# Kernel optimization log

Hardware: AMD Instinct MI355X
Metric: run time of the kernel (lower is better)

## Reference

```python
import jax, jax.numpy as jnp
import numpy as np

N_NODES = 50000
N_EDGES = 800000
D_IN = 128
D_OUT = 128


def setup_inputs() -> dict:
    key = jax.random.key(0)
    ks = jax.random.split(key, 10)
    x = jax.random.normal(ks[0], (N_NODES, D_IN), dtype=jnp.float32)
    lp_rows = jax.random.randint(ks[1], (N_EDGES,), 0, N_NODES, dtype=jnp.int32)
    lp_cols = jax.random.randint(ks[2], (N_EDGES,), 0, N_NODES, dtype=jnp.int32)
    # low-pass operator: positive normalized-adjacency-like weights
    lp_vals = jax.random.uniform(ks[3], (N_EDGES,), dtype=jnp.float32) / 16.0
    hp_rows = jax.random.randint(ks[4], (N_EDGES,), 0, N_NODES, dtype=jnp.int32)
    hp_cols = jax.random.randint(ks[5], (N_EDGES,), 0, N_NODES, dtype=jnp.int32)
    # high-pass operator: signed (Laplacian-like) weights
    hp_vals = jax.random.normal(ks[6], (N_EDGES,), dtype=jnp.float32) / 16.0
    alpha_w = jax.random.normal(ks[7], (1, D_IN), dtype=jnp.float32) * 0.05
    alpha_b = jnp.zeros((1,), dtype=jnp.float32)
    W = jax.random.normal(ks[8], (D_OUT, D_IN), dtype=jnp.float32) * (1.0 / np.sqrt(D_IN))
    b = jnp.zeros((D_OUT,), dtype=jnp.float32)
    return {"x": x, "lp_rows": lp_rows, "lp_cols": lp_cols, "lp_vals": lp_vals,
            "hp_rows": hp_rows, "hp_cols": hp_cols, "hp_vals": hp_vals,
            "alpha_w": alpha_w, "alpha_b": alpha_b, "W": W, "b": b}


def _spmm(rows, cols, vals, x, n):
    # COO sparse-dense matmul: out[r] += vals[e] * x[cols[e]]
    return jax.ops.segment_sum(vals[:, None] * x[cols], rows, num_segments=n)


def reference(x, lp_rows, lp_cols, lp_vals, hp_rows, hp_cols, hp_vals,
              alpha_w, alpha_b, W, b):
    n = x.shape[0]
    # per-node mixing gate: alpha_i = sigmoid(x_i . theta + b)  -> [N, 1]
    alpha = jax.nn.sigmoid(x @ alpha_w.T + alpha_b)
    z_lp = _spmm(lp_rows, lp_cols, lp_vals, x, n)   # [N, D_IN]
    z_hp = _spmm(hp_rows, hp_cols, hp_vals, x, n)   # [N, D_IN]
    z_mix = alpha * z_lp + (1.0 - alpha) * z_hp
    out = jax.nn.relu(z_mix @ W.T + b)              # use_activation=True
    return out, alpha
```

## Files before the change

kernel.cpp:

```cpp
#include <hip/hip_runtime.h>

#define N_NODES_C 50000
#define N_EDGES_C 800000
#define N_EDGES2_C (2 * N_EDGES_C)
#define D 128
#define NSHARD 8
#define OFCAP 4096

#define BROWS 4
#define NBKT (N_NODES_C / BROWS)
#define NSB (NSHARD * NBKT)
#define BCAP 32

#define GNODES 64
#define LDP 132
#define GGRID ((N_NODES_C + GNODES - 1) / GNODES)
#define FGRID 2048
#define FEPB ((N_EDGES2_C + FGRID - 1) / FGRID)
#define TOTG (GGRID + FGRID)

static __device__ __forceinline__ unsigned short f2bf(float f) {
  unsigned u = __float_as_uint(f);
  u += 0x7fff + ((u >> 16) & 1);
  return (unsigned short)(u >> 16);
}
static __device__ __forceinline__ float bf_lo(unsigned u) {
  return __uint_as_float(u << 16);
}
static __device__ __forceinline__ float bf_hi(unsigned u) {
  return __uint_as_float(u & 0xffff0000u);
}

static __device__ __forceinline__ int xcd_id() {
  int v;
  asm volatile("s_getreg_b32 %0, hwreg(HW_REG_XCC_ID, 0, 4)" : "=s"(v));
  return v & (NSHARD - 1);
}

__global__ __launch_bounds__(256) void alpha_zero_kernel(
    const float* __restrict__ x,
    const float* __restrict__ aw,
    const float* __restrict__ ab,
    float* __restrict__ alpha_out,
    float* __restrict__ alpha_ws,
    int* __restrict__ bcursor,
    int n) {
  int gtid = blockIdx.x * blockDim.x + threadIdx.x;
  if (gtid < NSB + 64) bcursor[gtid] = 0;

  int wave = gtid >> 6;
  int lane = threadIdx.x & 63;
  if (wave >= n) return;
  const float* xr = x + (size_t)wave * D;
  float s = xr[lane] * aw[lane] + xr[lane + 64] * aw[lane + 64];
  #pragma unroll
  for (int off = 32; off > 0; off >>= 1)
    s += __shfl_down(s, off);
  if (lane == 0) {
    float a = 1.0f / (1.0f + __expf(-(s + ab[0])));
    alpha_out[wave] = a;
    alpha_ws[wave] = a;
  }
}

__global__ __launch_bounds__(256) void gemm_fill_kernel(
    const float* __restrict__ x,
    const float* __restrict__ W,
    unsigned* __restrict__ y,
    const int* __restrict__ lp_rows, const int* __restrict__ lp_cols,
    const float* __restrict__ lp_vals,
    const int* __restrict__ hp_rows, const int* __restrict__ hp_cols,
    const float* __restrict__ hp_vals,
    const float* __restrict__ alpha,
    int* __restrict__ bcursor,
    uint2* __restrict__ bins,
    int* __restrict__ ofcnt,
    uint2* __restrict__ ofl,
    int n) {
  __shared__ float zs[GNODES][LDP];
  __shared__ float wt[64][LDP];

  int t = threadIdx.x;
  int bid = blockIdx.x;
  int g = (bid * GGRID) / TOTG;
  int gn = ((bid + 1) * GGRID) / TOTG;

  if (gn > g) {
    int node0 = g * GNODES;
    int tn = t & 15;
    int tjg = t >> 4;
    int jb = tjg * 4;

    #pragma unroll
    for (int it = 0; it < 8; ++it) {
      int f = t + it * 256;
      int r = f >> 5;
      int c4 = f & 31;
      int node = node0 + r;
      float4 v = make_float4(0.f, 0.f, 0.f, 0.f);
      if (node < n) v = ((const float4*)(x + (size_t)node * D))[c4];
      *(float4*)&zs[r][c4 * 4] = v;
    }

    for (int jh = 0; jh < 2; ++jh) {
      if (jh) __syncthreads();
      #pragma unroll
      for (int it = 0; it < 8; ++it) {
        int f = t + it * 256;
        int j = f >> 5;
        int k4 = f & 31;
        *(float4*)&wt[j][k4 * 4] =
            ((const float4*)W)[(size_t)(jh * 64 + j) * 32 + k4];
      }
      __syncthreads();

      float acc[4][4] = {};
      #pragma unroll 2
      for (int k = 0; k < D; k += 4) {
        float4 w0 = *(const float4*)&wt[jb + 0][k];
        float4 w1 = *(const float4*)&wt[jb + 1][k];
        float4 w2 = *(const float4*)&wt[jb + 2][k];
        float4 w3 = *(const float4*)&wt[jb + 3][k];
        float4 z0 = *(const float4*)&zs[tn][k];
        float4 z1 = *(const float4*)&zs[tn + 16][k];
        float4 z2 = *(const float4*)&zs[tn + 32][k];
        float4 z3 = *(const float4*)&zs[tn + 48][k];
        acc[0][0] += z0.x*w0.x + z0.y*w0.y + z0.z*w0.z + z0.w*w0.w;
        acc[0][1] += z0.x*w1.x + z0.y*w1.y + z0.z*w1.z + z0.w*w1.w;
        acc[0][2] += z0.x*w2.x + z0.y*w2.y + z0.z*w2.z + z0.w*w2.w;
        acc[0][3] += z0.x*w3.x + z0.y*w3.y + z0.z*w3.z + z0.w*w3.w;
        acc[1][0] += z1.x*w0.x + z1.y*w0.y + z1.z*w0.z + z1.w*w0.w;
        acc[1][1] += z1.x*w1.x + z1.y*w1.y + z1.z*w1.z + z1.w*w1.w;
        acc[1][2] += z1.x*w2.x + z1.y*w2.y + z1.z*w2.z + z1.w*w2.w;
        acc[1][3] += z1.x*w3.x + z1.y*w3.y + z1.z*w3.z + z1.w*w3.w;
        acc[2][0] += z2.x*w0.x + z2.y*w0.y + z2.z*w0.z + z2.w*w0.w;
        acc[2][1] += z2.x*w1.x + z2.y*w1.y + z2.z*w1.z + z2.w*w1.w;
        acc[2][2] += z2.x*w2.x + z2.y*w2.y + z2.z*w2.z + z2.w*w2.w;
        acc[2][3] += z2.x*w3.x + z2.y*w3.y + z2.z*w3.z + z2.w*w3.w;
        acc[3][0] += z3.x*w0.x + z3.y*w0.y + z3.z*w0.z + z3.w*w0.w;
        acc[3][1] += z3.x*w1.x + z3.y*w1.y + z3.z*w1.z + z3.w*w1.w;
        acc[3][2] += z3.x*w2.x + z3.y*w2.y + z3.z*w2.z + z3.w*w2.w;
        acc[3][3] += z3.x*w3.x + z3.y*w3.y + z3.z*w3.z + z3.w*w3.w;
      }

      #pragma unroll
      for (int ii = 0; ii < 4; ++ii) {
        int node = node0 + ii * 16 + tn;
        if (node < n) {
          uint2 o;
          o.x = (unsigned)f2bf(acc[ii][0]) | ((unsigned)f2bf(acc[ii][1]) << 16);
          o.y = (unsigned)f2bf(acc[ii][2]) | ((unsigned)f2bf(acc[ii][3]) << 16);
          *(uint2*)&y[(size_t)node * 64 + jh * 32 + tjg * 2] = o;
        }
      }
    }
  } else {
    int fb = bid - g;
    int xcc = xcd_id();
    int e0 = fb * FEPB;
    int e1 = e0 + FEPB;
    if (e1 > N_EDGES2_C) e1 = N_EDGES2_C;
    for (int e = e0 + t; e < e1; e += 256) {
      int r, c;
      float v;
      if (e < N_EDGES_C) {
        r = __builtin_nontemporal_load(lp_rows + e);
        c = __builtin_nontemporal_load(lp_cols + e);
        v = __builtin_nontemporal_load(lp_vals + e) * alpha[r];
      } else {
        int i = e - N_EDGES_C;
        r = __builtin_nontemporal_load(hp_rows + i);
        c = __builtin_nontemporal_load(hp_cols + i);
        v = __builtin_nontemporal_load(hp_vals + i) * (1.0f - alpha[r]);
      }
      int sb = xcc * NBKT + (r >> 2);
      int p = atomicAdd(&bcursor[sb], 1);
      if (p < BCAP) {
        bins[(size_t)sb * BCAP + p] =
            make_uint2(((unsigned)r << 16) | (unsigned)c, __float_as_uint(v));
      } else {
        int q = atomicAdd(ofcnt, 1);
        if (q < OFCAP)
          ofl[q] = make_uint2(((unsigned)r << 16) | (unsigned)c,
                              (unsigned)__float_as_int(v));
      }
    }
  }
}

__global__ __launch_bounds__(256) void gather_kernel(
    const int* __restrict__ bcursor,
    const uint2* __restrict__ bins,
    const unsigned* __restrict__ y,
    const float* __restrict__ bias,
    const int* __restrict__ ofcnt,
    const uint2* __restrict__ ofl,
    float* __restrict__ out) {
  int t = threadIdx.x;
  int w = t >> 6;
  int lane = t & 63;
  int bkt = blockIdx.x * 4 + w;

  float a0L = 0.f, a0H = 0.f, a1L = 0.f, a1H = 0.f;
  float a2L = 0.f, a2H = 0.f, a3L = 0.f, a3H = 0.f;

  #define ACC(RR, VV, UU)                                        \
    do {                                                         \
      float uL_ = bf_lo(UU), uH_ = bf_hi(UU);                    \
      switch (RR) {                                              \
        case 0: a0L += (VV) * uL_; a0H += (VV) * uH_; break;     \
        case 1: a1L += (VV) * uL_; a1H += (VV) * uH_; break;     \
        case 2: a2L += (VV) * uL_; a2H += (VV) * uH_; break;     \
        default: a3L += (VV) * uL_; a3H += (VV) * uH_; break;    \
      }                                                          \
    } while (0)

  int cnts[8];
  uint2 wvs[8];
  #pragma unroll
  for (int s = 0; s < 8; ++s) {
    int c = bcursor[s * NBKT + bkt];
    cnts[s] = c > BCAP ? BCAP : c;
  }
  #pragma unroll
  for (int s = 0; s < 8; ++s) {
    wvs[s] = make_uint2(0u, 0u);
    if (lane < cnts[s])
      wvs[s] = bins[(size_t)(s * NBKT + bkt) * BCAP + lane];
  }

  #pragma unroll
  for (int s = 0; s < 8; ++s) {
    int cnt = cnts[s];
    uint2 wv = wvs[s];
    int i = 0;
    for (; i + 7 < cnt; i += 8) {
      unsigned xk0 = (unsigned)__shfl((int)wv.x, i + 0);
      unsigned xk1 = (unsigned)__shfl((int)wv.x, i + 1);
      unsigned xk2 = (unsigned)__shfl((int)wv.x, i + 2);
      unsigned xk3 = (unsigned)__shfl((int)wv.x, i + 3);
      unsigned xk4 = (unsigned)__shfl((int)wv.x, i + 4);
      unsigned xk5 = (unsigned)__shfl((int)wv.x, i + 5);
      unsigned xk6 = (unsigned)__shfl((int)wv.x, i + 6);
      unsigned xk7 = (unsigned)__shfl((int)wv.x, i + 7);
      float v0 = __uint_as_float((unsigned)__shfl((int)wv.y, i + 0));
      float v1 = __uint_as_float((unsigned)__shfl((int)wv.y, i + 1));
      float v2 = __uint_as_float((unsigned)__shfl((int)wv.y, i + 2));
      float v3 = __uint_as_float((unsigned)__shfl((int)wv.y, i + 3));
      float v4 = __uint_as_float((unsigned)__shfl((int)wv.y, i + 4));
      float v5 = __uint_as_float((unsigned)__shfl((int)wv.y, i + 5));
      float v6 = __uint_as_float((unsigned)__shfl((int)wv.y, i + 6));
      float v7 = __uint_as_float((unsigned)__shfl((int)wv.y, i + 7));
      unsigned u0 = y[(size_t)(xk0 & 0xffffu) * 64 + lane];
      unsigned u1 = y[(size_t)(xk1 & 0xffffu) * 64 + lane];
      unsigned u2 = y[(size_t)(xk2 & 0xffffu) * 64 + lane];
      unsigned u3 = y[(size_t)(xk3 & 0xffffu) * 64 + lane];
      unsigned u4 = y[(size_t)(xk4 & 0xffffu) * 64 + lane];
      unsigned u5 = y[(size_t)(xk5 & 0xffffu) * 64 + lane];
      unsigned u6 = y[(size_t)(xk6 & 0xffffu) * 64 + lane];
      unsigned u7 = y[(size_t)(xk7 & 0xffffu) * 64 + lane];
      int r0 = (int)__builtin_amdgcn_readfirstlane((xk0 >> 16) & 3);
      int r1 = (int)__builtin_amdgcn_readfirstlane((xk1 >> 16) & 3);
      int r2 = (int)__builtin_amdgcn_readfirstlane((xk2 >> 16) & 3);
      int r3 = (int)__builtin_amdgcn_readfirstlane((xk3 >> 16) & 3);
      int r4 = (int)__builtin_amdgcn_readfirstlane((xk4 >> 16) & 3);
      int r5 = (int)__builtin_amdgcn_readfirstlane((xk5 >> 16) & 3);
      int r6 = (int)__builtin_amdgcn_readfirstlane((xk6 >> 16) & 3);
      int r7 = (int)__builtin_amdgcn_readfirstlane((xk7 >> 16) & 3);
      ACC(r0, v0, u0);
      ACC(r1, v1, u1);
      ACC(r2, v2, u2);
      ACC(r3, v3, u3);
      ACC(r4, v4, u4);
      ACC(r5, v5, u5);
      ACC(r6, v6, u6);
      ACC(r7, v7, u7);
    }
    for (; i + 3 < cnt; i += 4) {
      unsigned xk0 = (unsigned)__shfl((int)wv.x, i + 0);
      unsigned xk1 = (unsigned)__shfl((int)wv.x, i + 1);
      unsigned xk2 = (unsigned)__shfl((int)wv.x, i + 2);
      unsigned xk3 = (unsigned)__shfl((int)wv.x, i + 3);
      float v0 = __uint_as_float((unsigned)__shfl((int)wv.y, i + 0));
      float v1 = __uint_as_float((unsigned)__shfl((int)wv.y, i + 1));
      float v2 = __uint_as_float((unsigned)__shfl((int)wv.y, i + 2));
      float v3 = __uint_as_float((unsigned)__shfl((int)wv.y, i + 3));
      unsigned u0 = y[(size_t)(xk0 & 0xffffu) * 64 + lane];
      unsigned u1 = y[(size_t)(xk1 & 0xffffu) * 64 + lane];
      unsigned u2 = y[(size_t)(xk2 & 0xffffu) * 64 + lane];
      unsigned u3 = y[(size_t)(xk3 & 0xffffu) * 64 + lane];
      int r0 = (int)__builtin_amdgcn_readfirstlane((xk0 >> 16) & 3);
      int r1 = (int)__builtin_amdgcn_readfirstlane((xk1 >> 16) & 3);
      int r2 = (int)__builtin_amdgcn_readfirstlane((xk2 >> 16) & 3);
      int r3 = (int)__builtin_amdgcn_readfirstlane((xk3 >> 16) & 3);
      ACC(r0, v0, u0);
      ACC(r1, v1, u1);
      ACC(r2, v2, u2);
      ACC(r3, v3, u3);
    }
    for (; i < cnt; ++i) {
      unsigned xk0 = (unsigned)__shfl((int)wv.x, i);
      float v0 = __uint_as_float((unsigned)__shfl((int)wv.y, i));
      unsigned u0 = y[(size_t)(xk0 & 0xffffu) * 64 + lane];
      int r0 = (int)__builtin_amdgcn_readfirstlane((xk0 >> 16) & 3);
      ACC(r0, v0, u0);
    }
  }

  int nof = *ofcnt;
  if (nof > OFCAP) nof = OFCAP;
  for (int i = 0; i < nof; ++i) {
    uint2 o = ofl[i];
    unsigned r = o.x >> 16;
    if ((int)(r >> 2) == bkt) {
      unsigned u = y[(size_t)(o.x & 0xffffu) * 64 + lane];
      float v = __uint_as_float(o.y);
      ACC((int)(r & 3), v, u);
    }
  }
  #undef ACC

  float2 bv = *(const float2*)&bias[lane * 2];
  size_t ro = (size_t)bkt * 4 * D + lane * 2;
  float2 o0, o1, o2, o3;
  o0.x = fmaxf(a0L + bv.x, 0.0f); o0.y = fmaxf(a0H + bv.y, 0.0f);
  o1.x = fmaxf(a1L + bv.x, 0.0f); o1.y = fmaxf(a1H + bv.y, 0.0f);
  o2.x = fmaxf(a2L + bv.x, 0.0f); o2.y = fmaxf(a2H + bv.y, 0.0f);
  o3.x = fmaxf(a3L + bv.x, 0.0f); o3.y = fmaxf(a3H + bv.y, 0.0f);
  *(float2*)&out[ro + 0 * D] = o0;
  *(float2*)&out[ro + 1 * D] = o1;
  *(float2*)&out[ro + 2 * D] = o2;
  *(float2*)&out[ro + 3 * D] = o3;
}

extern "C" void kernel_launch(void* const* d_in, const int* in_sizes, int n_in,
                              void* d_out, int out_size, void* d_ws, size_t ws_size,
                              hipStream_t stream) {
  const float* x = (const float*)d_in[0];
  const int* lp_rows = (const int*)d_in[1];
  const int* lp_cols = (const int*)d_in[2];
  const float* lp_vals = (const float*)d_in[3];
  const int* hp_rows = (const int*)d_in[4];
  const int* hp_cols = (const int*)d_in[5];
  const float* hp_vals = (const float*)d_in[6];
  const float* alpha_w = (const float*)d_in[7];
  const float* alpha_b = (const float*)d_in[8];
  const float* W = (const float*)d_in[9];
  const float* bias = (const float*)d_in[10];

  float* out = (float*)d_out;
  float* alpha_out = out + (size_t)N_NODES_C * D;

  char* ws = (char*)d_ws;
  unsigned* y = (unsigned*)ws;   ws += (size_t)N_NODES_C * 64 * 4;
  float* alpha_ws = (float*)ws;  ws += 200192;
  int* bcursor = (int*)ws;       ws += (size_t)NSB * 4;
  int* ofcnt = (int*)ws;         ws += 256;
  uint2* ofl = (uint2*)ws;       ws += (size_t)OFCAP * 8;
  uint2* bins = (uint2*)ws;
  ws += (size_t)NSB * BCAP * 8;

  alpha_zero_kernel<<<(N_NODES_C + 3) / 4, 256, 0, stream>>>(
      x, alpha_w, alpha_b, alpha_out, alpha_ws, bcursor, N_NODES_C);

  gemm_fill_kernel<<<TOTG, 256, 0, stream>>>(
      x, W, y,
      lp_rows, lp_cols, lp_vals, hp_rows, hp_cols, hp_vals,
      alpha_ws, bcursor, bins, ofcnt, ofl, N_NODES_C);

  gather_kernel<<<NBKT / 4, 256, 0, stream>>>(
      bcursor, bins, (const unsigned*)y, bias, ofcnt, ofl, out);
}
```

Before: 272.5 us.

## Fuse alpha gate into gather and tag edge type in value LSB

Removes the per-node alpha computation from the first kernel and instead computes alpha inside the gather kernel, which keeps separate low-pass and high-pass accumulators per row and mixes them at the end. The edge type is encoded in the low mantissa bit of the stored weight, so the fill phase no longer does a random alpha[r] load per edge. The zero kernel becomes a small vectorized memset. The costs are doubled accumulator registers in the gather kernel, a wider per-edge switch, one lost mantissa bit in each weight, and a re-read of x rows in the gather kernel.

```diff
diff --git a/kernel.cpp b/kernel.cpp
--- a/kernel.cpp
+++ b/kernel.cpp
@@ -37,30 +37,9 @@
   return v & (NSHARD - 1);
 }
 
-__global__ __launch_bounds__(256) void alpha_zero_kernel(
-    const float* __restrict__ x,
-    const float* __restrict__ aw,
-    const float* __restrict__ ab,
-    float* __restrict__ alpha_out,
-    float* __restrict__ alpha_ws,
-    int* __restrict__ bcursor,
-    int n) {
-  int gtid = blockIdx.x * blockDim.x + threadIdx.x;
-  if (gtid < NSB + 64) bcursor[gtid] = 0;
-
-  int wave = gtid >> 6;
-  int lane = threadIdx.x & 63;
-  if (wave >= n) return;
-  const float* xr = x + (size_t)wave * D;
-  float s = xr[lane] * aw[lane] + xr[lane + 64] * aw[lane + 64];
-  #pragma unroll
-  for (int off = 32; off > 0; off >>= 1)
-    s += __shfl_down(s, off);
-  if (lane == 0) {
-    float a = 1.0f / (1.0f + __expf(-(s + ab[0])));
-    alpha_out[wave] = a;
-    alpha_ws[wave] = a;
-  }
+__global__ __launch_bounds__(256) void zero_kernel(int4* __restrict__ p) {
+  int g = blockIdx.x * 256 + threadIdx.x;
+  if (g < (NSB + 64) / 4) p[g] = make_int4(0, 0, 0, 0);
 }
 
 __global__ __launch_bounds__(256) void gemm_fill_kernel(
@@ -71,7 +50,6 @@
     const float* __restrict__ lp_vals,
     const int* __restrict__ hp_rows, const int* __restrict__ hp_cols,
     const float* __restrict__ hp_vals,
-    const float* __restrict__ alpha,
     int* __restrict__ bcursor,
     uint2* __restrict__ bins,
     int* __restrict__ ofcnt,
@@ -162,27 +140,26 @@
     if (e1 > N_EDGES2_C) e1 = N_EDGES2_C;
     for (int e = e0 + t; e < e1; e += 256) {
       int r, c;
-      float v;
+      unsigned vb;
       if (e < N_EDGES_C) {
         r = __builtin_nontemporal_load(lp_rows + e);
         c = __builtin_nontemporal_load(lp_cols + e);
-        v = __builtin_nontemporal_load(lp_vals + e) * alpha[r];
+        vb = (__float_as_uint(__builtin_nontemporal_load(lp_vals + e)) & ~1u) | 1u;
       } else {
         int i = e - N_EDGES_C;
         r = __builtin_nontemporal_load(hp_rows + i);
         c = __builtin_nontemporal_load(hp_cols + i);
-        v = __builtin_nontemporal_load(hp_vals + i) * (1.0f - alpha[r]);
+        vb = __float_as_uint(__builtin_nontemporal_load(hp_vals + i)) & ~1u;
       }
       int sb = xcc * NBKT + (r >> 2);
       int p = atomicAdd(&bcursor[sb], 1);
       if (p < BCAP) {
         bins[(size_t)sb * BCAP + p] =
-            make_uint2(((unsigned)r << 16) | (unsigned)c, __float_as_uint(v));
+            make_uint2(((unsigned)r << 16) | (unsigned)c, vb);
       } else {
         int q = atomicAdd(ofcnt, 1);
         if (q < OFCAP)
-          ofl[q] = make_uint2(((unsigned)r << 16) | (unsigned)c,
-                              (unsigned)__float_as_int(v));
+          ofl[q] = make_uint2(((unsigned)r << 16) | (unsigned)c, vb);
       }
     }
   }
@@ -193,27 +170,39 @@
     const uint2* __restrict__ bins,
     const unsigned* __restrict__ y,
     const float* __restrict__ bias,
+    const float* __restrict__ x,
+    const float* __restrict__ aw,
+    const float* __restrict__ ab,
     const int* __restrict__ ofcnt,
     const uint2* __restrict__ ofl,
-    float* __restrict__ out) {
+    float* __restrict__ out,
+    float* __restrict__ alpha_out) {
   int t = threadIdx.x;
   int w = t >> 6;
   int lane = t & 63;
   int bkt = blockIdx.x * 4 + w;
 
-  float a0L = 0.f, a0H = 0.f, a1L = 0.f, a1H = 0.f;
-  float a2L = 0.f, a2H = 0.f, a3L = 0.f, a3H = 0.f;
-
-  #define ACC(RR, VV, UU)                                        \
+  float l0L = 0.f, l0H = 0.f, l1L = 0.f, l1H = 0.f;
+  float l2L = 0.f, l2H = 0.f, l3L = 0.f, l3H = 0.f;
+  float h0L = 0.f, h0H = 0.f, h1L = 0.f, h1H = 0.f;
+  float h2L = 0.f, h2H = 0.f, h3L = 0.f, h3H = 0.f;
+
+  #define ACC(TAG, VV, UU)                                       \
     do {                                                         \
       float uL_ = bf_lo(UU), uH_ = bf_hi(UU);                    \
-      switch (RR) {                                              \
-        case 0: a0L += (VV) * uL_; a0H += (VV) * uH_; break;     \
-        case 1: a1L += (VV) * uL_; a1H += (VV) * uH_; break;     \
-        case 2: a2L += (VV) * uL_; a2H += (VV) * uH_; break;     \
-        default: a3L += (VV) * uL_; a3H += (VV) * uH_; break;    \
+      switch (TAG) {                                             \
+        case 0: h0L += (VV) * uL_; h0H += (VV) * uH_; break;     \
+        case 1: h1L += (VV) * uL_; h1H += (VV) * uH_; break;     \
+        case 2: h2L += (VV) * uL_; h2H += (VV) * uH_; break;     \
+        case 3: h3L += (VV) * uL_; h3H += (VV) * uH_; break;     \
+        case 4: l0L += (VV) * uL_; l0H += (VV) * uH_; break;     \
+        case 5: l1L += (VV) * uL_; l1H += (VV) * uH_; break;     \
+        case 6: l2L += (VV) * uL_; l2H += (VV) * uH_; break;     \
+        default: l3L += (VV) * uL_; l3H += (VV) * uH_; break;    \
       }                                                          \
     } while (0)
+  #define TAG_OF(XK, VB) \
+    ((int)__builtin_amdgcn_readfirstlane((((VB) & 1u) << 2) | (((XK) >> 16) & 3)))
 
   int cnts[8];
   uint2 wvs[8];
@@ -243,14 +232,14 @@
       unsigned xk5 = (unsigned)__shfl((int)wv.x, i + 5);
       unsigned xk6 = (unsigned)__shfl((int)wv.x, i + 6);
       unsigned xk7 = (unsigned)__shfl((int)wv.x, i + 7);
-      float v0 = __uint_as_float((unsigned)__shfl((int)wv.y, i + 0));
-      float v1 = __uint_as_float((unsigned)__shfl((int)wv.y, i + 1));
-      float v2 = __uint_as_float((unsigned)__shfl((int)wv.y, i + 2));
-      float v3 = __uint_as_float((unsigned)__shfl((int)wv.y, i + 3));
-      float v4 = __uint_as_float((unsigned)__shfl((int)wv.y, i + 4));
-      float v5 = __uint_as_float((unsigned)__shfl((int)wv.y, i + 5));
-      float v6 = __uint_as_float((unsigned)__shfl((int)wv.y, i + 6));
-      float v7 = __uint_as_float((unsigned)__shfl((int)wv.y, i + 7));
+      unsigned vb0 = (unsigned)__shfl((int)wv.y, i + 0);
+      unsigned vb1 = (unsigned)__shfl((int)wv.y, i + 1);
+      unsigned vb2 = (unsigned)__shfl((int)wv.y, i + 2);
+      unsigned vb3 = (unsigned)__shfl((int)wv.y, i + 3);
+      unsigned vb4 = (unsigned)__shfl((int)wv.y, i + 4);
+      unsigned vb5 = (unsigned)__shfl((int)wv.y, i + 5);
+      unsigned vb6 = (unsigned)__shfl((int)wv.y, i + 6);
+      unsigned vb7 = (unsigned)__shfl((int)wv.y, i + 7);
       unsigned u0 = y[(size_t)(xk0 & 0xffffu) * 64 + lane];
       unsigned u1 = y[(size_t)(xk1 & 0xffffu) * 64 + lane];
       unsigned u2 = y[(size_t)(xk2 & 0xffffu) * 64 + lane];
@@ -259,51 +248,38 @@
       unsigned u5 = y[(size_t)(xk5 & 0xffffu) * 64 + lane];
       unsigned u6 = y[(size_t)(xk6 & 0xffffu) * 64 + lane];
       unsigned u7 = y[(size_t)(xk7 & 0xffffu) * 64 + lane];
-      int r0 = (int)__builtin_amdgcn_readfirstlane((xk0 >> 16) & 3);
-      int r1 = (int)__builtin_amdgcn_readfirstlane((xk1 >> 16) & 3);
-      int r2 = (int)__builtin_amdgcn_readfirstlane((xk2 >> 16) & 3);
-      int r3 = (int)__builtin_amdgcn_readfirstlane((xk3 >> 16) & 3);
-      int r4 = (int)__builtin_amdgcn_readfirstlane((xk4 >> 16) & 3);
-      int r5 = (int)__builtin_amdgcn_readfirstlane((xk5 >> 16) & 3);
-      int r6 = (int)__builtin_amdgcn_readfirstlane((xk6 >> 16) & 3);
-      int r7 = (int)__builtin_amdgcn_readfirstlane((xk7 >> 16) & 3);
-      ACC(r0, v0, u0);
-      ACC(r1, v1, u1);
-      ACC(r2, v2, u2);
-      ACC(r3, v3, u3);
-      ACC(r4, v4, u4);
-      ACC(r5, v5, u5);
-      ACC(r6, v6, u6);
-      ACC(r7, v7, u7);
+      ACC(TAG_OF(xk0, vb0), __uint_as_float(vb0 & ~1u), u0);
+      ACC(TAG_OF(xk1, vb1), __uint_as_float(vb1 & ~1u), u1);
+      ACC(TAG_OF(xk2, vb2), __uint_as_float(vb2 & ~1u), u2);
+      ACC(TAG_OF(xk3, vb3), __uint_as_float(vb3 & ~1u), u3);
+      ACC(TAG_OF(xk4, vb4), __uint_as_float(vb4 & ~1u), u4);
+      ACC(TAG_OF(xk5, vb5), __uint_as_float(vb5 & ~1u), u5);
+      ACC(TAG_OF(xk6, vb6), __uint_as_float(vb6 & ~1u), u6);
+      ACC(TAG_OF(xk7, vb7), __uint_as_float(vb7 & ~1u), u7);
     }
     for (; i + 3 < cnt; i += 4) {
       unsigned xk0 = (unsigned)__shfl((int)wv.x, i + 0);
       unsigned xk1 = (unsigned)__shfl((int)wv.x, i + 1);
       unsigned xk2 = (unsigned)__shfl((int)wv.x, i + 2);
       unsigned xk3 = (unsigned)__shfl((int)wv.x, i + 3);
-      float v0 = __uint_as_float((unsigned)__shfl((int)wv.y, i + 0));
-      float v1 = __uint_as_float((unsigned)__shfl((int)wv.y, i + 1));
-      float v2 = __uint_as_float((unsigned)__shfl((int)wv.y, i + 2));
-      float v3 = __uint_as_float((unsigned)__shfl((int)wv.y, i + 3));
+      unsigned vb0 = (unsigned)__shfl((int)wv.y, i + 0);
+      unsigned vb1 = (unsigned)__shfl((int)wv.y, i + 1);
+      unsigned vb2 = (unsigned)__shfl((int)wv.y, i + 2);
+      unsigned vb3 = (unsigned)__shfl((int)wv.y, i + 3);
       unsigned u0 = y[(size_t)(xk0 & 0xffffu) * 64 + lane];
       unsigned u1 = y[(size_t)(xk1 & 0xffffu) * 64 + lane];
       unsigned u2 = y[(size_t)(xk2 & 0xffffu) * 64 + lane];
       unsigned u3 = y[(size_t)(xk3 & 0xffffu) * 64 + lane];
-      int r0 = (int)__builtin_amdgcn_readfirstlane((xk0 >> 16) & 3);
-      int r1 = (int)__builtin_amdgcn_readfirstlane((xk1 >> 16) & 3);
-      int r2 = (int)__builtin_amdgcn_readfirstlane((xk2 >> 16) & 3);
-      int r3 = (int)__builtin_amdgcn_readfirstlane((xk3 >> 16) & 3);
-      ACC(r0, v0, u0);
-      ACC(r1, v1, u1);
-      ACC(r2, v2, u2);
-      ACC(r3, v3, u3);
+      ACC(TAG_OF(xk0, vb0), __uint_as_float(vb0 & ~1u), u0);
+      ACC(TAG_OF(xk1, vb1), __uint_as_float(vb1 & ~1u), u1);
+      ACC(TAG_OF(xk2, vb2), __uint_as_float(vb2 & ~1u), u2);
+      ACC(TAG_OF(xk3, vb3), __uint_as_float(vb3 & ~1u), u3);
     }
     for (; i < cnt; ++i) {
       unsigned xk0 = (unsigned)__shfl((int)wv.x, i);
-      float v0 = __uint_as_float((unsigned)__shfl((int)wv.y, i));
+      unsigned vb0 = (unsigned)__shfl((int)wv.y, i);
       unsigned u0 = y[(size_t)(xk0 & 0xffffu) * 64 + lane];
-      int r0 = (int)__builtin_amdgcn_readfirstlane((xk0 >> 16) & 3);
-      ACC(r0, v0, u0);
+      ACC(TAG_OF(xk0, vb0), __uint_as_float(vb0 & ~1u), u0);
     }
   }
 
@@ -314,19 +290,44 @@
     unsigned r = o.x >> 16;
     if ((int)(r >> 2) == bkt) {
       unsigned u = y[(size_t)(o.x & 0xffffu) * 64 + lane];
-      float v = __uint_as_float(o.y);
-      ACC((int)(r & 3), v, u);
+      ACC((int)(((o.y & 1u) << 2) | (r & 3)), __uint_as_float(o.y & ~1u), u);
     }
   }
   #undef ACC
+  #undef TAG_OF
+
+  float awL = aw[lane], awH = aw[lane + 64];
+  float bb = ab[0];
+  const float* xr = x + (size_t)bkt * 4 * D;
+  float s0 = xr[0 * D + lane] * awL + xr[0 * D + lane + 64] * awH;
+  float s1 = xr[1 * D + lane] * awL + xr[1 * D + lane + 64] * awH;
+  float s2 = xr[2 * D + lane] * awL + xr[2 * D + lane + 64] * awH;
+  float s3 = xr[3 * D + lane] * awL + xr[3 * D + lane + 64] * awH;
+  #pragma unroll
+  for (int off = 32; off > 0; off >>= 1) {
+    s0 += __shfl_down(s0, off);
+    s1 += __shfl_down(s1, off);
+    s2 += __shfl_down(s2, off);
+    s3 += __shfl_down(s3, off);
+  }
+  float a0 = 1.0f / (1.0f + __expf(-(__shfl(s0, 0) + bb)));
+  float a1 = 1.0f / (1.0f + __expf(-(__shfl(s1, 0) + bb)));
+  float a2 = 1.0f / (1.0f + __expf(-(__shfl(s2, 0) + bb)));
+  float a3 = 1.0f / (1.0f + __expf(-(__shfl(s3, 0) + bb)));
+  if (lane == 0)
+    *(float4*)&alpha_out[(size_t)bkt * 4] = make_float4(a0, a1, a2, a3);
 
   float2 bv = *(const float2*)&bias[lane * 2];
   size_t ro = (size_t)bkt * 4 * D + lane * 2;
   float2 o0, o1, o2, o3;
-  o0.x = fmaxf(a0L + bv.x, 0.0f); o0.y = fmaxf(a0H + bv.y, 0.0f);
-  o1.x = fmaxf(a1L + bv.x, 0.0f); o1.y = fmaxf(a1H + bv.y, 0.0f);
-  o2.x = fmaxf(a2L + bv.x, 0.0f); o2.y = fmaxf(a2H + bv.y, 0.0f);
-  o3.x = fmaxf(a3L + bv.x, 0.0f); o3.y = fmaxf(a3H + bv.y, 0.0f);
+  o0.x = fmaxf(a0 * l0L + (1.f - a0) * h0L + bv.x, 0.0f);
+  o0.y = fmaxf(a0 * l0H + (1.f - a0) * h0H + bv.y, 0.0f);
+  o1.x = fmaxf(a1 * l1L + (1.f - a1) * h1L + bv.x, 0.0f);
+  o1.y = fmaxf(a1 * l1H + (1.f - a1) * h1H + bv.y, 0.0f);
+  o2.x = fmaxf(a2 * l2L + (1.f - a2) * h2L + bv.x, 0.0f);
+  o2.y = fmaxf(a2 * l2H + (1.f - a2) * h2H + bv.y, 0.0f);
+  o3.x = fmaxf(a3 * l3L + (1.f - a3) * h3L + bv.x, 0.0f);
+  o3.y = fmaxf(a3 * l3H + (1.f - a3) * h3H + bv.y, 0.0f);
   *(float2*)&out[ro + 0 * D] = o0;
   *(float2*)&out[ro + 1 * D] = o1;
   *(float2*)&out[ro + 2 * D] = o2;
@@ -359,15 +360,17 @@
   uint2* ofl = (uint2*)ws;       ws += (size_t)OFCAP * 8;
   uint2* bins = (uint2*)ws;
   ws += (size_t)NSB * BCAP * 8;
-
-  alpha_zero_kernel<<<(N_NODES_C + 3) / 4, 256, 0, stream>>>(
-      x, alpha_w, alpha_b, alpha_out, alpha_ws, bcursor, N_NODES_C);
+  (void)alpha_ws;
+
+  zero_kernel<<<((NSB + 64) / 4 + 255) / 256, 256, 0, stream>>>(
+      (int4*)bcursor);
 
   gemm_fill_kernel<<<TOTG, 256, 0, stream>>>(
       x, W, y,
       lp_rows, lp_cols, lp_vals, hp_rows, hp_cols, hp_vals,
-      alpha_ws, bcursor, bins, ofcnt, ofl, N_NODES_C);
+      bcursor, bins, ofcnt, ofl, N_NODES_C);
 
   gather_kernel<<<NBKT / 4, 256, 0, stream>>>(
-      bcursor, bins, (const unsigned*)y, bias, ofcnt, ofl, out);
-}
+      bcursor, bins, (const unsigned*)y, bias, x, alpha_w, alpha_b,
+      ofcnt, ofl, out, alpha_out);
+}
```

Result: slower. 322.6 us (+18.4%).
